# Kernel tuning notes

Hardware: AMD Instinct MI355X
Metric: run time of the kernel (lower is better)

The kernel has to match this reference:

```python
import jax, jax.numpy as jnp
import numpy as np

N, E, U, R = 20000, 200000, 32, 64
NTYPES = 95
CUTOFF = 5.0
LN_EPS = 1e-5


def _init_linear(key, fan_in, fan_out, bias=True, dtype=jnp.float32):
    kw, kb = jax.random.split(key)
    bound = 1.0 / np.sqrt(fan_in)
    W = jax.random.uniform(kw, (fan_in, fan_out), dtype, -bound, bound)
    if not bias:
        return W
    b = jax.random.uniform(kb, (fan_out,), dtype, -bound, bound)
    return W, b


def setup_inputs() -> dict:
    key = jax.random.key(0)
    ks = jax.random.split(key, 20)
    f = jnp.float32
    Wd1, bd1 = _init_linear(ks[6], R, U)
    Wd2, bd2 = _init_linear(ks[7], R, U)
    Wd3, bd3 = _init_linear(ks[8], R, U)
    Wemb2, bemb2 = _init_linear(ks[9], 2 * U, U)
    Wemb3, bemb3 = _init_linear(ks[10], R, U)
    Ws1, bs1 = _init_linear(ks[11], U, 2 * U)
    Ws2, bs2 = _init_linear(ks[12], 2 * U, 3 * U)
    return {
        "node_type": jax.random.randint(ks[0], (N,), 0, NTYPES),
        "edge_attr": jax.random.normal(ks[1], (E, R), f),
        "bond_dist": jax.random.uniform(ks[2], (E,), f, 0.1, CUTOFF),
        "bond_vec": jax.random.normal(ks[3], (E, 3), f),
        "src": jax.random.randint(ks[4], (E,), 0, N),
        "dst": jax.random.randint(ks[5], (E,), 0, N),
        "emb_table": jax.random.normal(ks[13], (NTYPES, U), f),
        "Wd1": Wd1, "bd1": bd1, "Wd2": Wd2, "bd2": bd2, "Wd3": Wd3, "bd3": bd3,
        "Wemb2": Wemb2, "bemb2": bemb2, "Wemb3": Wemb3, "bemb3": bemb3,
        "Wt0": _init_linear(ks[14], U, U, bias=False),
        "Wt1": _init_linear(ks[15], U, U, bias=False),
        "Wt2": _init_linear(ks[16], U, U, bias=False),
        "Ws1": Ws1, "bs1": bs1, "Ws2": Ws2, "bs2": bs2,
        "ln_g": jnp.ones((U,), f), "ln_b": jnp.zeros((U,), f),
    }


def reference(node_type, edge_attr, bond_dist, bond_vec, src, dst,
              emb_table, Wd1, bd1, Wd2, bd2, Wd3, bd3,
              Wemb2, bemb2, Wemb3, bemb3, Wt0, Wt1, Wt2,
              Ws1, bs1, Ws2, bs2, ln_g, ln_b):
    act = jax.nn.silu
    dt = edge_attr.dtype
    Z = emb_table[node_type]                                        # [N,U]
    # cosine cutoff
    C = 0.5 * (jnp.cos(jnp.pi * bond_dist / CUTOFF) + 1.0) * (bond_dist <= CUTOFF).astype(dt)
    W1 = (edge_attr @ Wd1 + bd1) * C[:, None]                       # [E,U]
    W2 = (edge_attr @ Wd2 + bd2) * C[:, None]
    W3 = (edge_attr @ Wd3 + bd3) * C[:, None]
    v = bond_vec / jnp.linalg.norm(bond_vec, axis=1, keepdims=True)  # [E,3]
    eye = jnp.eye(3, dtype=dt)
    zero = jnp.zeros_like(v[:, 0])
    # vector_to_skewtensor
    A = jnp.stack([zero, -v[:, 2], v[:, 1],
                   v[:, 2], zero, -v[:, 0],
                   -v[:, 1], v[:, 0], zero], axis=1).reshape(-1, 3, 3)
    # vector_to_symtensor (outer product is already symmetric)
    t = v[:, :, None] * v[:, None, :]                               # [E,3,3]
    S = t - (jnp.trace(t, axis1=-2, axis2=-1) / 3.0)[:, None, None] * eye
    # edge message: Zij = emb2([v_src, v_dst])
    Zij = jnp.concatenate([Z[src], Z[dst]], axis=1) @ Wemb2 + bemb2  # [E,U]
    fI = Zij * W1  # Zij * new_radial_tensor weights, fused (same math)
    fA = Zij * W2
    fS = Zij * W3
    Iedge = fI[:, :, None, None] * eye                              # [E,U,3,3]
    Aedge = fA[:, :, None, None] * A[:, None, :, :]
    Sedge = fS[:, :, None, None] * S[:, None, :, :]
    seg = lambda x: jax.ops.segment_sum(x, dst, num_segments=N)
    Ie, Ae, Se = seg(Iedge), seg(Aedge), seg(Sedge)                 # [N,U,3,3]
    # tensor_norm + LayerNorm
    nrm = jnp.sum((Ie + Ae + Se) ** 2, axis=(-2, -1))               # [N,U]
    mu = jnp.mean(nrm, axis=-1, keepdims=True)
    var = jnp.mean((nrm - mu) ** 2, axis=-1, keepdims=True)
    nrm = (nrm - mu) / jnp.sqrt(var + LN_EPS) * ln_g + ln_b
    # per-channel linear mixing of tensor components
    Ie = jnp.einsum('nuij,uv->nvij', Ie, Wt0)
    Ae = jnp.einsum('nuij,uv->nvij', Ae, Wt1)
    Se = jnp.einsum('nuij,uv->nvij', Se, Wt2)
    nrm = act(nrm @ Ws1 + bs1)
    nrm = act(nrm @ Ws2 + bs2)                                      # [N,3U]
    nrm = nrm.reshape(nrm.shape[0], U, 3)
    X = (nrm[..., 0, None, None] * Ie
         + nrm[..., 1, None, None] * Ae
         + nrm[..., 2, None, None] * Se)                            # [N,U,3,3]
    edge_feat = edge_attr @ Wemb3 + bemb3                           # [E,U]
    return X, edge_feat
```

## Files before the change

### kernel.cpp

```cpp
#include <hip/hip_runtime.h>


#define NPB 8
#define EPW 8

__device__ inline void atomAddF(float* p, float v) {
#if defined(__HIP_PLATFORM_AMD__)
    unsafeAtomicAdd(p, v);
#else
    atomicAdd(p, v);
#endif
}

__global__ void ptype_kernel(const float* __restrict__ emb,
                             const float* __restrict__ We2,
                             const float* __restrict__ be2,
                             float* __restrict__ Pt1, float* __restrict__ Pt2) {
    const int c = threadIdx.x & 31;
    const int t8 = threadIdx.x >> 5;
    for (int tb = 0; tb < 95; tb += 8) {
        const int t = tb + t8;
        if (t < 95) {
            float p1 = 0.f, p2 = 0.f;
            for (int k = 0; k < 32; ++k) {
                const float z = emb[t * 32 + k];
                p1 = fmaf(z, We2[k * 32 + c], p1);
                p2 = fmaf(z, We2[(32 + k) * 32 + c], p2);
            }
            Pt1[t * 32 + c] = p1 + be2[c];
            Pt2[t * 32 + c] = p2;
        }
    }
}

__global__ void prep_zero(const int* __restrict__ nt,
                          const float* __restrict__ Pt1, const float* __restrict__ Pt2,
                          float* __restrict__ acc,
                          float* __restrict__ P1, float* __restrict__ P2, int N) {
    const int i = blockIdx.x * 256 + threadIdx.x;
    if (i < N * 320) acc[i] = 0.0f;
    if (i < N * 32) {
        const int n = i >> 5, c = i & 31;
        const int t = nt[n];
        P1[i] = Pt1[t * 32 + c];
        P2[i] = Pt2[t * 32 + c];
    }
}

__global__ __launch_bounds__(256) void edge_kernel(
    const float* __restrict__ edge_attr,
    const float* __restrict__ bond_dist,
    const float* __restrict__ bond_vec,
    const int*   __restrict__ src,
    const int*   __restrict__ dst,
    const float* __restrict__ Wd1, const float* __restrict__ bd1,
    const float* __restrict__ Wd2, const float* __restrict__ bd2,
    const float* __restrict__ Wd3, const float* __restrict__ bd3,
    const float* __restrict__ We3, const float* __restrict__ be3,
    const float* __restrict__ P1,
    const float* __restrict__ P2,
    float* __restrict__ acc,
    float* __restrict__ efeat,
    int E)
{
    __shared__ float sW[4][64][32];
    const int tid = threadIdx.x;
    for (int i = tid; i < 4 * 2048; i += 256) {
        const int m = i >> 11, r = i & 2047;
        const float* W = (m == 0) ? Wd1 : (m == 1) ? Wd2 : (m == 2) ? Wd3 : We3;
        sW[m][r >> 5][r & 31] = W[r];
    }
    __syncthreads();

    const int lane = tid & 63;
    const int c = lane & 31;
    const int h = lane >> 5;
    const float bd1r = bd1[c], bd2r = bd2[c], bd3r = bd3[c], be3r = be3[c];
    const float* wbase = &sW[0][h * 32][c];

    const int wid = __builtin_amdgcn_readfirstlane((blockIdx.x * 256 + tid) >> 6);
    const int nw = gridDim.x * 4;
    const int ngroups = (E + EPW - 1) / EPW;

    for (int g = wid; g < ngroups; g += nw) {
        const int base = g * EPW;

        float xr[EPW];
#pragma unroll
        for (int j = 0; j < EPW; ++j) {
            int e = base + j; if (e >= E) e = E - 1;
            xr[j] = edge_attr[(size_t)e * 64 + lane];
        }

        float A0[EPW], A1[EPW], A2[EPW], A3[EPW];
#pragma unroll
        for (int j = 0; j < EPW; ++j) { A0[j] = 0.f; A1[j] = 0.f; A2[j] = 0.f; A3[j] = 0.f; }

#pragma unroll 8
        for (int kk = 0; kk < 32; ++kk) {
            const float w0 = wbase[kk * 32];
            const float w1 = wbase[kk * 32 + 2048];
            const float w2 = wbase[kk * 32 + 4096];
            const float w3 = wbase[kk * 32 + 6144];
#pragma unroll
            for (int j = 0; j < EPW; ++j) {
                const float xb = __shfl(xr[j], kk, 32);
                A0[j] = fmaf(xb, w0, A0[j]);
                A1[j] = fmaf(xb, w1, A1[j]);
                A2[j] = fmaf(xb, w2, A2[j]);
                A3[j] = fmaf(xb, w3, A3[j]);
            }
        }

#pragma unroll
        for (int jj = 0; jj < 4; ++jj) {
            const float sd0 = h ? A0[jj] : A0[jj + 4];
            const float sd1 = h ? A1[jj] : A1[jj + 4];
            const float sd2 = h ? A2[jj] : A2[jj + 4];
            const float sd3 = h ? A3[jj] : A3[jj + 4];
            const float mn0 = h ? A0[jj + 4] : A0[jj];
            const float mn1 = h ? A1[jj + 4] : A1[jj];
            const float mn2 = h ? A2[jj + 4] : A2[jj];
            const float mn3 = h ? A3[jj + 4] : A3[jj];
            const float t0 = mn0 + __shfl_xor(sd0, 32);
            const float t1 = mn1 + __shfl_xor(sd1, 32);
            const float t2 = mn2 + __shfl_xor(sd2, 32);
            const float t3 = mn3 + __shfl_xor(sd3, 32);

            const int e = base + jj + 4 * h;
            const bool val = (e < E);
            const int ec = val ? e : (E - 1);

            const float d = bond_dist[ec];
            const float C = (d <= 5.0f) ? 0.5f * (cosf(3.14159265358979323846f * d / 5.0f) + 1.0f) : 0.0f;
            float v0 = bond_vec[3 * (size_t)ec + 0];
            float v1 = bond_vec[3 * (size_t)ec + 1];
            float v2 = bond_vec[3 * (size_t)ec + 2];
            const float inv = 1.0f / sqrtf(v0 * v0 + v1 * v1 + v2 * v2);
            v0 *= inv; v1 *= inv; v2 *= inv;
            const float tr3 = (v0 * v0 + v1 * v1 + v2 * v2) * (1.0f / 3.0f);
            const float y00 = v0 * v0 - tr3, y11 = v1 * v1 - tr3, y22 = v2 * v2 - tr3;
            const float y01 = v0 * v1, y02 = v0 * v2, y12 = v1 * v2;

            const int si = src[ec], di = dst[ec];
            const float az = P1[(size_t)si * 32 + c] + P2[(size_t)di * 32 + c];

            const float a1v = t0 + bd1r;
            const float a2v = t1 + bd2r;
            const float a3v = t2 + bd3r;
            const float a4v = t3 + be3r;
            const float w1v = a1v * C, w2v = a2v * C, w3v = a3v * C;
            const float fI = az * w1v, fA = az * w2v, fS = az * w3v;

            if (val) {
                efeat[(size_t)e * 32 + c] = a4v;
                float* ap = acc + (size_t)di * 320 + c;
                atomAddF(ap,       fI);
                atomAddF(ap + 32,  fA * v0);
                atomAddF(ap + 64,  fA * v1);
                atomAddF(ap + 96,  fA * v2);
                atomAddF(ap + 128, fS * y00);
                atomAddF(ap + 160, fS * y01);
                atomAddF(ap + 192, fS * y02);
                atomAddF(ap + 224, fS * y11);
                atomAddF(ap + 256, fS * y12);
                atomAddF(ap + 288, fS * y22);
            }
        }
    }
}

__global__ __launch_bounds__(256) void node_kernel(
    const float* __restrict__ acc,
    const float* __restrict__ Wt0, const float* __restrict__ Wt1, const float* __restrict__ Wt2,
    const float* __restrict__ Ws1, const float* __restrict__ bs1,
    const float* __restrict__ Ws2, const float* __restrict__ bs2,
    const float* __restrict__ lng, const float* __restrict__ lnb,
    float* __restrict__ xout,
    int N)
{
    __shared__ float wt[3][32][32];
    __shared__ float ws1[32][64];
    __shared__ float ws2[64][96];
    __shared__ float sb1[64], sb2[96], sg[32], sbv[32];
    __shared__ float accS[NPB][10][32];
    __shared__ float nrmS[NPB][32];
    __shared__ float h1S[NPB][64];

    const int tid = threadIdx.x;
    for (int i = tid; i < 1024; i += 256) wt[0][i >> 5][i & 31] = Wt0[i];
    for (int i = tid; i < 1024; i += 256) wt[1][i >> 5][i & 31] = Wt1[i];
    for (int i = tid; i < 1024; i += 256) wt[2][i >> 5][i & 31] = Wt2[i];
    for (int i = tid; i < 2048; i += 256) ws1[i >> 6][i & 63] = Ws1[i];
    for (int i = tid; i < 6144; i += 256) ws2[i / 96][i % 96] = Ws2[i];
    if (tid < 64) sb1[tid] = bs1[tid];
    if (tid < 96) sb2[tid] = bs2[tid];
    if (tid < 32) { sg[tid] = lng[tid]; sbv[tid] = lnb[tid]; }
    __syncthreads();

    const int ln_ = tid >> 5, u = tid & 31;
    const int n = blockIdx.x * NPB + ln_;
    const bool valid = n < N;

    float c0 = 0, a0 = 0, a1 = 0, a2 = 0, s00 = 0, s01 = 0, s02 = 0, s11 = 0, s12 = 0, s22 = 0;
    if (valid) {
        const float* ap = acc + (size_t)n * 320 + u;
        c0 = ap[0];  a0 = ap[32];  a1 = ap[64];  a2 = ap[96];
        s00 = ap[128]; s01 = ap[160]; s02 = ap[192];
        s11 = ap[224]; s12 = ap[256]; s22 = ap[288];
    }
    accS[ln_][0][u] = c0;  accS[ln_][1][u] = a0;  accS[ln_][2][u] = a1;  accS[ln_][3][u] = a2;
    accS[ln_][4][u] = s00; accS[ln_][5][u] = s01; accS[ln_][6][u] = s02;
    accS[ln_][7][u] = s11; accS[ln_][8][u] = s12; accS[ln_][9][u] = s22;

    float m00 = c0 + s00, m11 = c0 + s11, m22 = c0 + s22;
    float nrm = m00 * m00 + m11 * m11 + m22 * m22
              + 2.0f * (s01 * s01 + a2 * a2 + s02 * s02 + a1 * a1 + s12 * s12 + a0 * a0);

    float sum = nrm;
#pragma unroll
    for (int o = 16; o >= 1; o >>= 1) sum += __shfl_xor(sum, o, 32);
    float mu = sum * (1.0f / 32.0f);
    float dv = nrm - mu;
    float vs = dv * dv;
#pragma unroll
    for (int o = 16; o >= 1; o >>= 1) vs += __shfl_xor(vs, o, 32);
    float var = vs * (1.0f / 32.0f);
    float nl = dv * rsqrtf(var + 1e-5f) * sg[u] + sbv[u];
    nrmS[ln_][u] = nl;
    __syncthreads();

    float h1a = sb1[u], h1b = sb1[u + 32];
#pragma unroll
    for (int k = 0; k < 32; ++k) {
        float x = nrmS[ln_][k];
        h1a += x * ws1[k][u];
        h1b += x * ws1[k][u + 32];
    }
    h1a = h1a / (1.0f + __expf(-h1a));
    h1b = h1b / (1.0f + __expf(-h1b));
    h1S[ln_][u] = h1a; h1S[ln_][u + 32] = h1b;
    __syncthreads();

    float f0 = sb2[3 * u], f1 = sb2[3 * u + 1], f2 = sb2[3 * u + 2];
#pragma unroll
    for (int k = 0; k < 64; ++k) {
        float hh = h1S[ln_][k];
        f0 += hh * ws2[k][3 * u];
        f1 += hh * ws2[k][3 * u + 1];
        f2 += hh * ws2[k][3 * u + 2];
    }
    f0 = f0 / (1.0f + __expf(-f0));
    f1 = f1 / (1.0f + __expf(-f1));
    f2 = f2 / (1.0f + __expf(-f2));

    float m0 = 0, ma0 = 0, ma1 = 0, ma2 = 0;
    float ms00 = 0, ms01 = 0, ms02 = 0, ms11 = 0, ms12 = 0, ms22 = 0;
#pragma unroll
    for (int k = 0; k < 32; ++k) {
        float w0 = wt[0][k][u], w1 = wt[1][k][u], w2 = wt[2][k][u];
        m0   += accS[ln_][0][k] * w0;
        ma0  += accS[ln_][1][k] * w1;
        ma1  += accS[ln_][2][k] * w1;
        ma2  += accS[ln_][3][k] * w1;
        ms00 += accS[ln_][4][k] * w2;
        ms01 += accS[ln_][5][k] * w2;
        ms02 += accS[ln_][6][k] * w2;
        ms11 += accS[ln_][7][k] * w2;
        ms12 += accS[ln_][8][k] * w2;
        ms22 += accS[ln_][9][k] * w2;
    }
    if (valid) {
        float* xp = xout + (size_t)n * 288 + u * 9;
        xp[0] = f0 * m0 + f2 * ms00;
        xp[1] = f1 * (-ma2) + f2 * ms01;
        xp[2] = f1 * ( ma1) + f2 * ms02;
        xp[3] = f1 * ( ma2) + f2 * ms01;
        xp[4] = f0 * m0 + f2 * ms11;
        xp[5] = f1 * (-ma0) + f2 * ms12;
        xp[6] = f1 * (-ma1) + f2 * ms02;
        xp[7] = f1 * ( ma0) + f2 * ms12;
        xp[8] = f0 * m0 + f2 * ms22;
    }
}

extern "C" void kernel_launch(void* const* d_in, const int* in_sizes, int n_in,
                              void* d_out, int out_size, void* d_ws, size_t ws_size,
                              hipStream_t stream) {
    const int N = in_sizes[0];
    const int E = in_sizes[2];

    float* acc = (float*)d_ws;
    float* P1  = acc + (size_t)N * 320;
    float* P2  = P1 + (size_t)N * 32;
    float* Pt1 = P2 + (size_t)N * 32;
    float* Pt2 = Pt1 + 95 * 32;

    float* xout  = (float*)d_out;
    float* efeat = xout + (size_t)N * 288;

    ptype_kernel<<<1, 256, 0, stream>>>(
        (const float*)d_in[6], (const float*)d_in[13], (const float*)d_in[14], Pt1, Pt2);

    prep_zero<<<(N * 320 + 255) / 256, 256, 0, stream>>>(
        (const int*)d_in[0], Pt1, Pt2, acc, P1, P2, N);

    edge_kernel<<<1024, 256, 0, stream>>>(
        (const float*)d_in[1], (const float*)d_in[2], (const float*)d_in[3],
        (const int*)d_in[4], (const int*)d_in[5],
        (const float*)d_in[7],  (const float*)d_in[8],
        (const float*)d_in[9],  (const float*)d_in[10],
        (const float*)d_in[11], (const float*)d_in[12],
        (const float*)d_in[15], (const float*)d_in[16],
        P1, P2, acc, efeat, E);

    node_kernel<<<(N + NPB - 1) / NPB, 256, 0, stream>>>(
        acc,
        (const float*)d_in[17], (const float*)d_in[18], (const float*)d_in[19],
        (const float*)d_in[20], (const float*)d_in[21],
        (const float*)d_in[22], (const float*)d_in[23],
        (const float*)d_in[24], (const float*)d_in[25],
        xout, N);
}
```

Measured before the change: 428.3 us.

## Make node kernel persistent, vectorize shared layouts, parallelize ptype and retune edge grid

The node kernel becomes a grid-stride persistent kernel with 512 blocks, so the shared-memory weight staging is paid once per block rather than once per 8-node group. The per-node accumulators are kept in shared memory as float4 triples and the three Wt matrices are packed into one array, allowing vector LDS reads in the mixing loop. The ptype kernel is spread over 12 blocks instead of running serially in one, and the edge kernel grid grows from 1024 to 1280 blocks. The trade-off is an extra barrier per group iteration and fewer resident blocks to hide latency in the node kernel.

```diff
diff --git a/kernel.cpp b/kernel.cpp
--- a/kernel.cpp
+++ b/kernel.cpp
@@ -17,19 +17,16 @@
                              const float* __restrict__ be2,
                              float* __restrict__ Pt1, float* __restrict__ Pt2) {
     const int c = threadIdx.x & 31;
-    const int t8 = threadIdx.x >> 5;
-    for (int tb = 0; tb < 95; tb += 8) {
-        const int t = tb + t8;
-        if (t < 95) {
-            float p1 = 0.f, p2 = 0.f;
-            for (int k = 0; k < 32; ++k) {
-                const float z = emb[t * 32 + k];
-                p1 = fmaf(z, We2[k * 32 + c], p1);
-                p2 = fmaf(z, We2[(32 + k) * 32 + c], p2);
-            }
-            Pt1[t * 32 + c] = p1 + be2[c];
-            Pt2[t * 32 + c] = p2;
-        }
+    const int t = blockIdx.x * 8 + (threadIdx.x >> 5);
+    if (t < 95) {
+        float p1 = 0.f, p2 = 0.f;
+        for (int k = 0; k < 32; ++k) {
+            const float z = emb[t * 32 + k];
+            p1 = fmaf(z, We2[k * 32 + c], p1);
+            p2 = fmaf(z, We2[(32 + k) * 32 + c], p2);
+        }
+        Pt1[t * 32 + c] = p1 + be2[c];
+        Pt2[t * 32 + c] = p2;
     }
 }
 
@@ -177,20 +174,23 @@
     const float* __restrict__ Ws2, const float* __restrict__ bs2,
     const float* __restrict__ lng, const float* __restrict__ lnb,
     float* __restrict__ xout,
-    int N)
+    int N, int ngroups)
 {
-    __shared__ float wt[3][32][32];
+    __shared__ float wtS[32][96];
     __shared__ float ws1[32][64];
     __shared__ float ws2[64][96];
     __shared__ float sb1[64], sb2[96], sg[32], sbv[32];
-    __shared__ float accS[NPB][10][32];
+    __shared__ float4 accS4[NPB][32][3];
     __shared__ float nrmS[NPB][32];
     __shared__ float h1S[NPB][64];
 
     const int tid = threadIdx.x;
-    for (int i = tid; i < 1024; i += 256) wt[0][i >> 5][i & 31] = Wt0[i];
-    for (int i = tid; i < 1024; i += 256) wt[1][i >> 5][i & 31] = Wt1[i];
-    for (int i = tid; i < 1024; i += 256) wt[2][i >> 5][i & 31] = Wt2[i];
+    for (int i = tid; i < 1024; i += 256) {
+        const int k = i >> 5, u = i & 31;
+        wtS[k][u]      = Wt0[i];
+        wtS[k][32 + u] = Wt1[i];
+        wtS[k][64 + u] = Wt2[i];
+    }
     for (int i = tid; i < 2048; i += 256) ws1[i >> 6][i & 63] = Ws1[i];
     for (int i = tid; i < 6144; i += 256) ws2[i / 96][i % 96] = Ws2[i];
     if (tid < 64) sb1[tid] = bs1[tid];
@@ -199,88 +199,95 @@
     __syncthreads();
 
     const int ln_ = tid >> 5, u = tid & 31;
-    const int n = blockIdx.x * NPB + ln_;
-    const bool valid = n < N;
-
-    float c0 = 0, a0 = 0, a1 = 0, a2 = 0, s00 = 0, s01 = 0, s02 = 0, s11 = 0, s12 = 0, s22 = 0;
-    if (valid) {
-        const float* ap = acc + (size_t)n * 320 + u;
-        c0 = ap[0];  a0 = ap[32];  a1 = ap[64];  a2 = ap[96];
-        s00 = ap[128]; s01 = ap[160]; s02 = ap[192];
-        s11 = ap[224]; s12 = ap[256]; s22 = ap[288];
-    }
-    accS[ln_][0][u] = c0;  accS[ln_][1][u] = a0;  accS[ln_][2][u] = a1;  accS[ln_][3][u] = a2;
-    accS[ln_][4][u] = s00; accS[ln_][5][u] = s01; accS[ln_][6][u] = s02;
-    accS[ln_][7][u] = s11; accS[ln_][8][u] = s12; accS[ln_][9][u] = s22;
-
-    float m00 = c0 + s00, m11 = c0 + s11, m22 = c0 + s22;
-    float nrm = m00 * m00 + m11 * m11 + m22 * m22
-              + 2.0f * (s01 * s01 + a2 * a2 + s02 * s02 + a1 * a1 + s12 * s12 + a0 * a0);
-
-    float sum = nrm;
-#pragma unroll
-    for (int o = 16; o >= 1; o >>= 1) sum += __shfl_xor(sum, o, 32);
-    float mu = sum * (1.0f / 32.0f);
-    float dv = nrm - mu;
-    float vs = dv * dv;
-#pragma unroll
-    for (int o = 16; o >= 1; o >>= 1) vs += __shfl_xor(vs, o, 32);
-    float var = vs * (1.0f / 32.0f);
-    float nl = dv * rsqrtf(var + 1e-5f) * sg[u] + sbv[u];
-    nrmS[ln_][u] = nl;
-    __syncthreads();
-
-    float h1a = sb1[u], h1b = sb1[u + 32];
-#pragma unroll
-    for (int k = 0; k < 32; ++k) {
-        float x = nrmS[ln_][k];
-        h1a += x * ws1[k][u];
-        h1b += x * ws1[k][u + 32];
-    }
-    h1a = h1a / (1.0f + __expf(-h1a));
-    h1b = h1b / (1.0f + __expf(-h1b));
-    h1S[ln_][u] = h1a; h1S[ln_][u + 32] = h1b;
-    __syncthreads();
-
-    float f0 = sb2[3 * u], f1 = sb2[3 * u + 1], f2 = sb2[3 * u + 2];
-#pragma unroll
-    for (int k = 0; k < 64; ++k) {
-        float hh = h1S[ln_][k];
-        f0 += hh * ws2[k][3 * u];
-        f1 += hh * ws2[k][3 * u + 1];
-        f2 += hh * ws2[k][3 * u + 2];
-    }
-    f0 = f0 / (1.0f + __expf(-f0));
-    f1 = f1 / (1.0f + __expf(-f1));
-    f2 = f2 / (1.0f + __expf(-f2));
-
-    float m0 = 0, ma0 = 0, ma1 = 0, ma2 = 0;
-    float ms00 = 0, ms01 = 0, ms02 = 0, ms11 = 0, ms12 = 0, ms22 = 0;
-#pragma unroll
-    for (int k = 0; k < 32; ++k) {
-        float w0 = wt[0][k][u], w1 = wt[1][k][u], w2 = wt[2][k][u];
-        m0   += accS[ln_][0][k] * w0;
-        ma0  += accS[ln_][1][k] * w1;
-        ma1  += accS[ln_][2][k] * w1;
-        ma2  += accS[ln_][3][k] * w1;
-        ms00 += accS[ln_][4][k] * w2;
-        ms01 += accS[ln_][5][k] * w2;
-        ms02 += accS[ln_][6][k] * w2;
-        ms11 += accS[ln_][7][k] * w2;
-        ms12 += accS[ln_][8][k] * w2;
-        ms22 += accS[ln_][9][k] * w2;
-    }
-    if (valid) {
-        float* xp = xout + (size_t)n * 288 + u * 9;
-        xp[0] = f0 * m0 + f2 * ms00;
-        xp[1] = f1 * (-ma2) + f2 * ms01;
-        xp[2] = f1 * ( ma1) + f2 * ms02;
-        xp[3] = f1 * ( ma2) + f2 * ms01;
-        xp[4] = f0 * m0 + f2 * ms11;
-        xp[5] = f1 * (-ma0) + f2 * ms12;
-        xp[6] = f1 * (-ma1) + f2 * ms02;
-        xp[7] = f1 * ( ma0) + f2 * ms12;
-        xp[8] = f0 * m0 + f2 * ms22;
+
+    for (int g = blockIdx.x; g < ngroups; g += gridDim.x) {
+        const int n = g * NPB + ln_;
+        const bool valid = n < N;
+
+        float c0 = 0, a0 = 0, a1 = 0, a2 = 0, s00 = 0, s01 = 0, s02 = 0, s11 = 0, s12 = 0, s22 = 0;
+        if (valid) {
+            const float* ap = acc + (size_t)n * 320 + u;
+            c0 = ap[0];  a0 = ap[32];  a1 = ap[64];  a2 = ap[96];
+            s00 = ap[128]; s01 = ap[160]; s02 = ap[192];
+            s11 = ap[224]; s12 = ap[256]; s22 = ap[288];
+        }
+        accS4[ln_][u][0] = make_float4(c0, a0, a1, a2);
+        accS4[ln_][u][1] = make_float4(s00, s01, s02, s11);
+        accS4[ln_][u][2] = make_float4(s12, s22, 0.f, 0.f);
+
+        const float m00 = c0 + s00, m11 = c0 + s11, m22 = c0 + s22;
+        float nrm = m00 * m00 + m11 * m11 + m22 * m22
+                  + 2.0f * (s01 * s01 + a2 * a2 + s02 * s02 + a1 * a1 + s12 * s12 + a0 * a0);
+
+        float sum = nrm;
+#pragma unroll
+        for (int o = 16; o >= 1; o >>= 1) sum += __shfl_xor(sum, o, 32);
+        const float mu = sum * (1.0f / 32.0f);
+        const float dv = nrm - mu;
+        float vs = dv * dv;
+#pragma unroll
+        for (int o = 16; o >= 1; o >>= 1) vs += __shfl_xor(vs, o, 32);
+        const float var = vs * (1.0f / 32.0f);
+        const float nl = dv * rsqrtf(var + 1e-5f) * sg[u] + sbv[u];
+        nrmS[ln_][u] = nl;
+        __syncthreads();
+
+        float h1a = sb1[u], h1b = sb1[u + 32];
+#pragma unroll
+        for (int k = 0; k < 32; ++k) {
+            const float x = nrmS[ln_][k];
+            h1a += x * ws1[k][u];
+            h1b += x * ws1[k][u + 32];
+        }
+        h1a = h1a / (1.0f + __expf(-h1a));
+        h1b = h1b / (1.0f + __expf(-h1b));
+        h1S[ln_][u] = h1a; h1S[ln_][u + 32] = h1b;
+        __syncthreads();
+
+        float f0 = sb2[3 * u], f1 = sb2[3 * u + 1], f2 = sb2[3 * u + 2];
+#pragma unroll
+        for (int k = 0; k < 64; ++k) {
+            const float hh = h1S[ln_][k];
+            f0 += hh * ws2[k][3 * u];
+            f1 += hh * ws2[k][3 * u + 1];
+            f2 += hh * ws2[k][3 * u + 2];
+        }
+        f0 = f0 / (1.0f + __expf(-f0));
+        f1 = f1 / (1.0f + __expf(-f1));
+        f2 = f2 / (1.0f + __expf(-f2));
+
+        float m0 = 0, ma0 = 0, ma1 = 0, ma2 = 0;
+        float ms00 = 0, ms01 = 0, ms02 = 0, ms11 = 0, ms12 = 0, ms22 = 0;
+#pragma unroll
+        for (int k = 0; k < 32; ++k) {
+            const float w0 = wtS[k][u], w1 = wtS[k][32 + u], w2 = wtS[k][64 + u];
+            const float4 q0 = accS4[ln_][k][0];
+            const float4 q1 = accS4[ln_][k][1];
+            const float4 q2 = accS4[ln_][k][2];
+            m0   += q0.x * w0;
+            ma0  += q0.y * w1;
+            ma1  += q0.z * w1;
+            ma2  += q0.w * w1;
+            ms00 += q1.x * w2;
+            ms01 += q1.y * w2;
+            ms02 += q1.z * w2;
+            ms11 += q1.w * w2;
+            ms12 += q2.x * w2;
+            ms22 += q2.y * w2;
+        }
+        if (valid) {
+            float* xp = xout + (size_t)n * 288 + u * 9;
+            xp[0] = f0 * m0 + f2 * ms00;
+            xp[1] = f1 * (-ma2) + f2 * ms01;
+            xp[2] = f1 * ( ma1) + f2 * ms02;
+            xp[3] = f1 * ( ma2) + f2 * ms01;
+            xp[4] = f0 * m0 + f2 * ms11;
+            xp[5] = f1 * (-ma0) + f2 * ms12;
+            xp[6] = f1 * (-ma1) + f2 * ms02;
+            xp[7] = f1 * ( ma0) + f2 * ms12;
+            xp[8] = f0 * m0 + f2 * ms22;
+        }
+        __syncthreads();
     }
 }
 
@@ -299,13 +306,13 @@
     float* xout  = (float*)d_out;
     float* efeat = xout + (size_t)N * 288;
 
-    ptype_kernel<<<1, 256, 0, stream>>>(
+    ptype_kernel<<<12, 256, 0, stream>>>(
         (const float*)d_in[6], (const float*)d_in[13], (const float*)d_in[14], Pt1, Pt2);
 
     prep_zero<<<(N * 320 + 255) / 256, 256, 0, stream>>>(
         (const int*)d_in[0], Pt1, Pt2, acc, P1, P2, N);
 
-    edge_kernel<<<1024, 256, 0, stream>>>(
+    edge_kernel<<<1280, 256, 0, stream>>>(
         (const float*)d_in[1], (const float*)d_in[2], (const float*)d_in[3],
         (const int*)d_in[4], (const int*)d_in[5],
         (const float*)d_in[7],  (const float*)d_in[8],
@@ -314,11 +321,12 @@
         (const float*)d_in[15], (const float*)d_in[16],
         P1, P2, acc, efeat, E);
 
-    node_kernel<<<(N + NPB - 1) / NPB, 256, 0, stream>>>(
+    const int ngroups = (N + NPB - 1) / NPB;
+    node_kernel<<<512, 256, 0, stream>>>(
         acc,
         (const float*)d_in[17], (const float*)d_in[18], (const float*)d_in[19],
         (const float*)d_in[20], (const float*)d_in[21],
         (const float*)d_in[22], (const float*)d_in[23],
         (const float*)d_in[24], (const float*)d_in[25],
-        xout, N);
-}
+        xout, N, ngroups);
+}
```

New measurement: 430.8 us. About the same (+0.6%).
